# Optimization experiments

Measured on AMD Instinct MI355X. Metric: run time of the kernel, lower is better.

The kernel has to match this reference:

```python
import jax, jax.numpy as jnp
from jax import lax
import numpy as np

B, L, D = 2048, 100, 64      # batch, max_len, embedding_dim
K = 64                       # embedding_num (codebook entries)
CB = K * 8                   # code_book_dim = 512 (== D*8 encoder out channels)
ITEMS = 1_000_000
EPS = 1e-3                   # tf.layers.batch_normalization default epsilon


def setup_inputs() -> dict:
    key = jax.random.key(0)
    ks = jax.random.split(key, 16)
    w = lambda i, shape: jax.random.normal(ks[i], shape, dtype=jnp.float32) * 0.05
    z = lambda c: jnp.zeros((c,), jnp.float32)
    o = lambda c: jnp.ones((c,), jnp.float32)
    return {
        "history_item_ids": jax.random.randint(ks[0], (B, L), 0, ITEMS, dtype=jnp.int32),
        "history_item_masks": jax.random.randint(ks[1], (B, L), 0, 2, dtype=jnp.int32),
        "item_embedding_table": jax.random.normal(ks[2], (ITEMS, D), dtype=jnp.float32),
        "user_book": jax.random.normal(ks[3], (K, CB), dtype=jnp.float32),
        "e_w1": w(4, (2, 2, D, 2 * D)), "e_b1": z(2 * D), "e_g1": o(2 * D), "e_be1": z(2 * D),
        "e_w2": w(5, (2, 2, 2 * D, 4 * D)), "e_b2": z(4 * D), "e_g2": o(4 * D), "e_be2": z(4 * D),
        "e_w3": w(6, (2, 2, 4 * D, 8 * D)), "e_b3": z(8 * D),
        "d_w1": w(7, (2, 2, 8 * D, 4 * D)), "d_b1": z(4 * D), "d_g1": o(4 * D), "d_be1": z(4 * D),
        "d_w2": w(8, (2, 2, 4 * D, 2 * D)), "d_b2": z(2 * D), "d_g2": o(2 * D), "d_be2": z(2 * D),
        "d_w3": w(9, (2, 2, 2 * D, D)), "d_b3": z(D),
    }


def _forward(history_item_ids, history_item_masks, item_embedding_table, user_book,
             e_w1, e_b1, e_g1, e_be1, e_w2, e_b2, e_g2, e_be2, e_w3, e_b3,
             d_w1, d_b1, d_g1, d_be1, d_w2, d_b2, d_g2, d_be2, d_w3, d_b3):
    dn = ('NHWC', 'HWIO', 'NHWC')
    bn = lambda x, g, b: x * (g / jnp.sqrt(1.0 + EPS)) + b  # inference BN: moving mean 0, var 1
    conv = lambda x, w_, b_: lax.conv_general_dilated(x, w_, (1, 1), 'VALID', dimension_numbers=dn) + b_
    deconv = lambda x, w_, b_: lax.conv_transpose(x, w_, (1, 1), 'VALID', dimension_numbers=dn) + b_

    mask = (history_item_masks >= 1).astype(jnp.float32)               # [B,L]
    hist = item_embedding_table[history_item_ids] * mask[..., None]    # [B,L,D]

    H = int(L ** 0.5); W = L // H
    h = hist.reshape(-1, H, W, D)
    h = jax.nn.relu(bn(conv(h, e_w1, e_b1), e_g1, e_be1))              # [B,9,9,2D]
    h = jax.nn.relu(bn(conv(h, e_w2, e_b2), e_g2, e_be2))              # [B,8,8,4D]
    x_encode = conv(h, e_w3, e_b3)                                     # [B,7,7,CB]

    # nearest-neighbor codebook lookup (get_quantized)
    flat = x_encode.reshape(-1, CB)                                    # [B*49,CB]
    dist = ((flat * flat).sum(1, keepdims=True)
            + (user_book * user_book).sum(1)
            - 2.0 * flat @ user_book.T)                                # [B*49,K]
    idx = jnp.argmin(dist, axis=1)
    quantized = user_book[idx].reshape(x_encode.shape)                 # [B,7,7,CB]

    # straight-through estimator
    st = x_encode + lax.stop_gradient(quantized - x_encode)
    g = jax.nn.relu(bn(deconv(st, d_w1, d_b1), d_g1, d_be1))           # [B,8,8,4D]
    g = jax.nn.relu(bn(deconv(g, d_w2, d_b2), d_g2, d_be2))            # [B,9,9,2D]
    vq_x = deconv(g, d_w3, d_b3).reshape(hist.shape)                   # [B,L,D]

    vq_mean = vq_x.sum(1) / mask.sum(-1, keepdims=True)                # [B,D]
    mse = lambda a, b: jnp.mean((a - b) ** 2)
    beta = 0.25
    vqvae_loss = (mse(hist, vq_x)
                  + mse(quantized, lax.stop_gradient(x_encode))
                  + beta * mse(x_encode, lax.stop_gradient(quantized)))
    return vq_mean, vq_x, vqvae_loss


def reference(history_item_ids, history_item_masks, item_embedding_table, user_book,
              e_w1, e_b1, e_g1, e_be1, e_w2, e_b2, e_g2, e_be2, e_w3, e_b3,
              d_w1, d_b1, d_g1, d_be1, d_w2, d_b2, d_g2, d_be2, d_w3, d_b3):
    return _forward(history_item_ids, history_item_masks, item_embedding_table, user_book,
                    e_w1, e_b1, e_g1, e_be1, e_w2, e_b2, e_g2, e_be2, e_w3, e_b3,
                    d_w1, d_b1, d_g1, d_be1, d_w2, d_b2, d_g2, d_be2, d_w3, d_b3)
```

## Files before the change

kernel.cpp:

```cpp
#include <hip/hip_runtime.h>
#include <hip/hip_bf16.h>
#include <cstdint>
#include <cstddef>


typedef __attribute__((ext_vector_type(8))) short short8v;
typedef __attribute__((ext_vector_type(4))) float f32x4;

constexpr int B  = 2048;
constexpr int L  = 100;
constexpr int K  = 64;
constexpr int CB = 512;
#define MARGIN 0.1f

constexpr size_t R0_OFF  = 0;
constexpr size_t R1_OFF  = 51380224;
constexpr size_t IDX_OFF = 84934656;
constexpr size_t CBN_OFF = 85035008;
constexpr size_t CNT_OFF = 85035072;
constexpr size_t ACC_OFF = 85035088;
constexpr size_t WL_OFF  = 85035104;
constexpr size_t WB_OFF  = 85135456;

constexpr size_t EW1H=0,       EW1L=32768;
constexpr size_t EW2H=65536,   EW2L=196608;
constexpr size_t EW3H=327680;
constexpr size_t DW2H=851968,  DW3H=983040;
constexpr size_t W3BH=1015808, W3BL=1081344;

constexpr size_t BW1_OFF  = WB_OFF + 573440;
constexpr size_t DOTB_OFF = BW1_OFF + 65536;

__device__ inline ushort bf16_hi(float f){ __hip_bfloat16 h=__float2bfloat16(f); return *(ushort*)&h; }
__device__ inline float  bf16_tof(ushort u){ __hip_bfloat16 h; *(ushort*)&h=u; return __bfloat162float(h); }

__device__ void wtrans(const float* __restrict__ w, int IC, int OC,
                       ushort* __restrict__ hi, ushort* __restrict__ lo,
                       int gid, int gsz)
{
    int tot = 4*IC*OC;
    for (int i = gid; i < tot; i += gsz) {
        int kk = i/(IC*OC), r = i - kk*(IC*OC), ic = r/OC, oc = r - ic*OC;
        float v = w[i];
        ushort h = bf16_hi(v);
        size_t dst = ((size_t)kk*OC + oc)*IC + ic;
        hi[dst] = h;
        if (lo) lo[dst] = bf16_hi(v - bf16_tof(h));
    }
}

__global__ __launch_bounds__(256)
void wprep_k(const float* e1, const float* e2, const float* e3,
             const float* d2, const float* d3, ushort* wb)
{
    int gid = blockIdx.x*256 + threadIdx.x, gsz = gridDim.x*256;
    wtrans(e1,  64, 128, wb+EW1H, wb+EW1L, gid, gsz);
    wtrans(e2, 128, 256, wb+EW2H, wb+EW2L, gid, gsz);
    wtrans(e3, 256, 512, wb+EW3H, nullptr, gid, gsz);
    wtrans(d2, 256, 128, wb+DW2H, nullptr, gid, gsz);
    wtrans(d3, 128,  64, wb+DW3H, nullptr, gid, gsz);
}

__global__ __launch_bounds__(256)
void w3b_k(const float* __restrict__ e_w3, const float* __restrict__ book,
           ushort* __restrict__ wb)
{
    const int kk = blockIdx.x >> 6, k = blockIdx.x & 63, ic = threadIdx.x;
    const float4* wr = (const float4*)(e_w3 + ((size_t)(kk*256)+ic)*512);
    const float4* br = (const float4*)(book + (size_t)k*512);
    float s = 0.f;
    for (int c = 0; c < 128; ++c) {
        float4 a = wr[c], bb = br[c];
        s = fmaf(a.x,bb.x,fmaf(a.y,bb.y,fmaf(a.z,bb.z,fmaf(a.w,bb.w,s))));
    }
    size_t dst = ((size_t)(kk*64+k))*256 + ic;
    ushort h = bf16_hi(s);
    wb[W3BH+dst] = h;
    wb[W3BL+dst] = bf16_hi(s - bf16_tof(h));
}

__global__ __launch_bounds__(256)
void bw1_k(const float* __restrict__ d_w1, const float* __restrict__ book,
           float* __restrict__ bw1)
{
    const int tap = blockIdx.x >> 6, k = blockIdx.x & 63, oc = threadIdx.x;
    const float* br = book + (size_t)k*512;
    const float* wr = d_w1 + (size_t)(tap*512)*256 + oc;
    float s = 0.f;
    for (int ic = 0; ic < 512; ++ic)
        s = fmaf(br[ic], wr[(size_t)ic*256], s);
    bw1[((size_t)(tap*64+k))*256 + oc] = s;
}

__global__ __launch_bounds__(256)
void prep_k(const float* __restrict__ book, const float* __restrict__ e_b3,
            float* __restrict__ cbn, float* __restrict__ dotb,
            float* __restrict__ acc, int* __restrict__ cnt)
{
    const int t = threadIdx.x;
    if (t < 64) {
        const float* r = book + t * 512;
        float s = 0.f, d = 0.f;
        for (int c = 0; c < 512; ++c) { s = fmaf(r[c], r[c], s); d = fmaf(e_b3[c], r[c], d); }
        cbn[t] = s; dotb[t] = d;
    }
    if (t == 64 || t == 65) acc[t-64] = 0.f;
    if (t == 66) *cnt = 0;
}

template<int IH,int IW,int IC,int OC,int PAD,int MODE,bool HASBN,bool SPLIT,
         int OCS,int ICC,int MT,int OUTFMT,bool FUSE,int SMP,bool DBUF>
__global__ __launch_bounds__(256)
void sconv_k(const uint* __restrict__ in_pk, const ushort* __restrict__ in_bf,
             const int* __restrict__ ids, const int* __restrict__ masks,
             const float* __restrict__ table,
             const ushort* __restrict__ wt_hi, const ushort* __restrict__ wt_lo,
             const float* __restrict__ bias, const float* __restrict__ gamma,
             const float* __restrict__ beta,
             float* __restrict__ out_f, uint* __restrict__ out_pk,
             ushort* __restrict__ out_bf, float* __restrict__ out_mean,
             float* __restrict__ acc_g)
{
    constexpr int OH=IH+2*PAD-1, OW=IW+2*PAD-1, NPOS=OH*OW, IHW=IH*IW;
    constexpr int OCB=OC/OCS, NPW=OCB/4, NT=NPW/16;
    constexpr int NCH=IC/ICC, KS=ICC/32;
    constexpr int PL=SPLIT?2:1;
    constexpr int NB=(DBUF && NCH>1)?2:1;
    constexpr int AROWS=IHW+1, RB=ICC*2;
    constexpr int C8=ICC/8;
    constexpr int NITEMS=SMP*IHW*C8;
    constexpr int SI=(NITEMS+255)/256;
    constexpr bool EXACT=(SI*256==NITEMS);
    constexpr int SPLB=AROWS*RB;
    constexpr int SAMB=PL*SPLB;
    constexpr int BUFB=SMP*SAMB;

    __shared__ ushort s_a[NB*SMP*PL*AROWS*ICC];
    char* sb=(char*)s_a;

    const int v=blockIdx.x, r8=v&7, iv=v>>3;
    const int b0 = (r8*(B/SMP/8) + iv/OCS)*SMP;
    const int sl = iv - (iv/OCS)*OCS;

    const int tid=threadIdx.x, lane=tid&63, wv=tid>>6;
    const int l15=lane&15, lq=lane>>4;
    const int n0=sl*OCB + wv*NPW;

    int arow[4][MT];
    #pragma unroll
    for(int kk=0;kk<4;++kk){
        const int ky=kk>>1, kx=kk&1;
        #pragma unroll
        for(int m=0;m<MT;++m){
            int p=m*16+l15;
            int py=p/OW, px=p-py*OW;
            int ty=py+ky-PAD, tx=px+kx-PAD;
            bool ok=(p<NPOS)&&((unsigned)ty<(unsigned)IH)&&((unsigned)tx<(unsigned)IW);
            arow[kk][m]= ok ? ty*IW+tx : IHW;
        }
    }

    f32x4 acc[SMP][MT][NT];
    #pragma unroll
    for(int s=0;s<SMP;++s)
        #pragma unroll
        for(int m=0;m<MT;++m)
            #pragma unroll
            for(int n=0;n<NT;++n) acc[s][m][n]=(f32x4)0.0f;

    uint4 r0[SI];
    uint4 r1[(MODE==1||MODE==3)?SI:1];
    float msk[(MODE==1)?SI:1];

    auto stage_load=[&](int c){
        const int ic0=c*ICC;
        #pragma unroll
        for(int t=0;t<SI;++t){
            int idx=tid+t*256;
            if(EXACT || idx<NITEMS){
                int row=idx/C8, g=idx-row*C8;
                int s=row/IHW, r=row-s*IHW;
                if constexpr(MODE==1){
                    int id=ids[(b0+s)*L+r];
                    msk[t]=(masks[(b0+s)*L+r]>=1)?1.f:0.f;
                    const float* src=table+(size_t)id*64+g*8;
                    r0[t]=*(const uint4*)src;
                    r1[t]=*(const uint4*)(src+4);
                } else if constexpr(MODE==3){
                    const uint* src=in_pk+((size_t)(b0+s)*IHW+r)*IC+ic0+g*8;
                    r0[t]=*(const uint4*)src;
                    r1[t]=*(const uint4*)(src+4);
                } else {
                    r0[t]=*(const uint4*)(in_bf+((size_t)(b0+s)*IHW+r)*IC+ic0+g*8);
                }
            }
        }
    };

    auto stage_write=[&](int bufb){
        #pragma unroll
        for(int t=0;t<SI;++t){
            int idx=tid+t*256;
            if(EXACT || idx<NITEMS){
                int row=idx/C8, g=idx-row*C8;
                int s=row/IHW, r=row-s*IHW;
                int boff=bufb + s*SAMB + r*RB + ((g^(r&7))<<4);
                if constexpr(MODE==1){
                    const float* f0=(const float*)&r0[t];
                    const float* f1=(const float*)&r1[t];
                    float vv[8]={f0[0]*msk[t],f0[1]*msk[t],f0[2]*msk[t],f0[3]*msk[t],
                                 f1[0]*msk[t],f1[1]*msk[t],f1[2]*msk[t],f1[3]*msk[t]};
                    ushort hh[8], ll[8];
                    #pragma unroll
                    for(int j=0;j<8;++j){ hh[j]=bf16_hi(vv[j]); ll[j]=bf16_hi(vv[j]-bf16_tof(hh[j])); }
                    *(uint4*)(sb+boff)=*(uint4*)hh;
                    *(uint4*)(sb+SPLB+boff)=*(uint4*)ll;
                } else if constexpr(MODE==3){
                    const uint* u0=(const uint*)&r0[t];
                    const uint* u1=(const uint*)&r1[t];
                    ushort hh[8], ll[8];
                    #pragma unroll
                    for(int j=0;j<4;++j){ hh[j]=(ushort)(u0[j]&0xffffu); ll[j]=(ushort)(u0[j]>>16); }
                    #pragma unroll
                    for(int j=0;j<4;++j){ hh[4+j]=(ushort)(u1[j]&0xffffu); ll[4+j]=(ushort)(u1[j]>>16); }
                    *(uint4*)(sb+boff)=*(uint4*)hh;
                    *(uint4*)(sb+SPLB+boff)=*(uint4*)ll;
                } else {
                    *(uint4*)(sb+boff)=r0[t];
                }
            }
        }
    };

    auto zero_rows=[&](){
        for(int z=tid; z<NB*SMP*PL*C8; z+=256){
            int nb=z/(SMP*PL*C8), rz=z-nb*(SMP*PL*C8);
            int s=rz/(PL*C8), rz2=rz-s*(PL*C8), pl=rz2/C8, g=rz2-pl*C8;
            *(uint4*)(sb + nb*BUFB + s*SAMB + pl*SPLB + IHW*RB + (g<<4)) = make_uint4(0,0,0,0);
        }
    };

    auto do_mfma=[&](int bufb, int c){
        const int ic0=c*ICC;
        __builtin_amdgcn_s_setprio(1);
        #pragma unroll
        for(int kk=0;kk<4;++kk){
            #pragma unroll
            for(int ks=0;ks<KS;++ks){
                short8v bhv[NT]; short8v blv[SPLIT?NT:1];
                #pragma unroll
                for(int n=0;n<NT;++n){
                    int col=n0+n*16+l15;
                    size_t widx=((size_t)kk*OC+col)*IC+ic0+ks*32+lq*8;
                    bhv[n]=*(const short8v*)(wt_hi+widx);
                    if constexpr(SPLIT) blv[n]=*(const short8v*)(wt_lo+widx);
                }
                #pragma unroll
                for(int s=0;s<SMP;++s){
                    const int sbase=bufb + s*SAMB;
                    #pragma unroll
                    for(int m=0;m<MT;++m){
                        int off=sbase + arow[kk][m]*RB + ((((ks<<2)|lq)^(arow[kk][m]&7))<<4);
                        short8v ah=*(const short8v*)(sb+off);
                        if constexpr(SPLIT){
                            short8v al=*(const short8v*)(sb+SPLB+off);
                            #pragma unroll
                            for(int n=0;n<NT;++n){
                                acc[s][m][n]=__builtin_amdgcn_mfma_f32_16x16x32_bf16(ah,bhv[n],acc[s][m][n],0,0,0);
                                acc[s][m][n]=__builtin_amdgcn_mfma_f32_16x16x32_bf16(ah,blv[n],acc[s][m][n],0,0,0);
                                acc[s][m][n]=__builtin_amdgcn_mfma_f32_16x16x32_bf16(al,bhv[n],acc[s][m][n],0,0,0);
                            }
                        } else {
                            #pragma unroll
                            for(int n=0;n<NT;++n)
                                acc[s][m][n]=__builtin_amdgcn_mfma_f32_16x16x32_bf16(ah,bhv[n],acc[s][m][n],0,0,0);
                        }
                    }
                }
            }
        }
        __builtin_amdgcn_s_setprio(0);
    };

    if constexpr(NB==1){
        stage_load(0);
        zero_rows();
        for(int c=0;c<NCH;++c){
            if(c) __syncthreads();
            stage_write(0);
            __syncthreads();
            if(c+1<NCH) stage_load(c+1);
            do_mfma(0,c);
        }
    } else {
        stage_load(0);
        stage_write(0);
        zero_rows();
        __syncthreads();
        for(int c=0;c<NCH;++c){
            if(c+1<NCH) stage_load(c+1);
            do_mfma((c&1)*BUFB,c);
            if(c+1<NCH){
                stage_write(((c+1)&1)*BUFB);
                __syncthreads();
            }
        }
    }

    const float rs=(float)(1.0/sqrt(1.0+1e-3));
    float lsum=0.f, colsum=0.f;
    #pragma unroll
    for(int s=0;s<SMP;++s){
        const int b=b0+s;
        #pragma unroll
        for(int n=0;n<NT;++n){
            int col=n0+n*16+l15;
            float bi=bias[col];
            float gsc=0.f, bt=0.f;
            if constexpr(HASBN){ gsc=gamma[col]*rs; bt=beta[col]; }
            #pragma unroll
            for(int m=0;m<MT;++m){
                #pragma unroll
                for(int j=0;j<4;++j){
                    int p=m*16+lq*4+j;
                    if(p<NPOS){
                        float vx=acc[s][m][n][j]+bi;
                        if constexpr(HASBN) vx=fmaxf(fmaf(vx,gsc,bt),0.f);
                        size_t g=(size_t)b*NPOS+p;
                        if constexpr(OUTFMT==0){
                            out_f[g*OC+col]=vx;
                        } else if constexpr(OUTFMT==1){
                            ushort h=bf16_hi(vx);
                            ushort lo=bf16_hi(vx-bf16_tof(h));
                            out_pk[g*OC+col]=(uint)h | ((uint)lo<<16);
                        } else {
                            out_bf[g*OC+col]=bf16_hi(vx);
                        }
                        if constexpr(FUSE){
                            int id=ids[b*L+p];
                            float mm=(masks[b*L+p]>=1)?1.f:0.f;
                            float h=table[(size_t)id*64+col]*mm;
                            float df=h-vx;
                            lsum=fmaf(df,df,lsum);
                            colsum+=vx;
                        }
                    }
                }
            }
        }
    }

    if constexpr(FUSE){
        const int b=b0;
        float mc=0.f;
        for(int l=lane;l<L;l+=64) mc += (masks[b*L+l]>=1)?1.f:0.f;
        #pragma unroll
        for(int off=32;off;off>>=1) mc+=__shfl_xor(mc,off);
        colsum += __shfl_xor(colsum,16);
        colsum += __shfl_xor(colsum,32);
        if(lq==0) out_mean[b*64 + n0 + l15] = colsum/mc;
        #pragma unroll
        for(int off=32;off;off>>=1) lsum+=__shfl_xor(lsum,off);
        __syncthreads();
        float* red=(float*)sb;
        if(lane==0) red[wv]=lsum;
        __syncthreads();
        if(tid==0) atomicAdd(acc_g+0, red[0]+red[1]+red[2]+red[3]);
    }
}

__device__ inline int xswz(int row, int sl){ return (sl ^ (row&31) ^ ((row>>3)&7)) << 4; }

__global__ __launch_bounds__(512)
void xnd4_k(const uint* __restrict__ in_pk,
            const ushort* __restrict__ wx,
            const ushort* __restrict__ w3bh, const ushort* __restrict__ w3bl,
            const float* __restrict__ xbias,
            const float* __restrict__ cbn, const float* __restrict__ dotb,
            int* __restrict__ qidx, float* __restrict__ acc_g,
            int* __restrict__ cnt, int* __restrict__ wl)
{
    constexpr int NPOS=49, OW=7, MT=4;
    constexpr int ROWB=512;
    constexpr int PLB=64*ROWB;

    __shared__ ushort s_a[2*64*256];
    char* sb=(char*)s_a;

    const int v=blockIdx.x;
    const int b=(v&7)*(B/8)+(v>>3);
    const int tid=threadIdx.x, lane=tid&63, wv=tid>>6;
    const int l15=lane&15, lq=lane>>4;

    #pragma unroll
    for(int t=0;t<4;++t){
        int idx=tid+t*512;
        int row=idx>>5, sl=idx&31;
        const uint* src=in_pk+((size_t)b*64+row)*256+sl*8;
        uint4 u0=*(const uint4*)src, u1=*(const uint4*)(src+4);
        const uint* p0=(const uint*)&u0;
        const uint* p1=(const uint*)&u1;
        ushort hh[8], ll[8];
        #pragma unroll
        for(int j=0;j<4;++j){ hh[j]=(ushort)(p0[j]&0xffffu); ll[j]=(ushort)(p0[j]>>16); }
        #pragma unroll
        for(int j=0;j<4;++j){ hh[4+j]=(ushort)(p1[j]&0xffffu); ll[4+j]=(ushort)(p1[j]>>16); }
        int boff=row*ROWB+xswz(row,sl);
        *(uint4*)(sb+boff)=*(uint4*)hh;
        *(uint4*)(sb+PLB+boff)=*(uint4*)ll;
    }
    __syncthreads();

    int arow[4][MT];
    #pragma unroll
    for(int kk=0;kk<4;++kk){
        const int ky=kk>>1, kx=kk&1;
        #pragma unroll
        for(int m=0;m<MT;++m){
            int p=m*16+l15;
            int py=p/OW, px=p-py*OW;
            arow[kk][m]= (p<NPOS) ? (py+ky)*8+(px+kx) : 0;
        }
    }

    f32x4 accd[MT];
    #pragma unroll
    for(int m=0;m<MT;++m) accd[m]=(f32x4)0.0f;
    if(wv<4){
        __builtin_amdgcn_s_setprio(1);
        #pragma unroll
        for(int kk=0;kk<4;++kk){
            #pragma unroll
            for(int ks=0;ks<8;++ks){
                int cold=wv*16+l15;
                size_t wdx=((size_t)kk*64+cold)*256+ks*32+lq*8;
                short8v bdh=*(const short8v*)(w3bh+wdx);
                short8v bdl=*(const short8v*)(w3bl+wdx);
                const int slb=ks*4+lq;
                #pragma unroll
                for(int m=0;m<MT;++m){
                    int r=arow[kk][m];
                    int off=r*ROWB+xswz(r,slb);
                    short8v ah=*(const short8v*)(sb+off);
                    short8v al=*(const short8v*)(sb+PLB+off);
                    accd[m]=__builtin_amdgcn_mfma_f32_16x16x32_bf16(ah,bdh,accd[m],0,0,0);
                    accd[m]=__builtin_amdgcn_mfma_f32_16x16x32_bf16(ah,bdl,accd[m],0,0,0);
                    accd[m]=__builtin_amdgcn_mfma_f32_16x16x32_bf16(al,bdh,accd[m],0,0,0);
                }
            }
        }
        __builtin_amdgcn_s_setprio(0);
    }

    float xs=0.f;
    #pragma unroll
    for(int cc=0;cc<2;++cc){
        f32x4 accx[MT][2];
        #pragma unroll
        for(int m=0;m<MT;++m){ accx[m][0]=(f32x4)0.0f; accx[m][1]=(f32x4)0.0f; }
        const int col0=wv*64+cc*32+l15;
        __builtin_amdgcn_s_setprio(1);
        #pragma unroll
        for(int kk=0;kk<4;++kk){
            #pragma unroll
            for(int ks=0;ks<8;++ks){
                short8v bx0=*(const short8v*)(wx+((size_t)kk*512+col0)*256+ks*32+lq*8);
                short8v bx1=*(const short8v*)(wx+((size_t)kk*512+col0+16)*256+ks*32+lq*8);
                const int slb=ks*4+lq;
                #pragma unroll
                for(int m=0;m<MT;++m){
                    int r=arow[kk][m];
                    int off=r*ROWB+xswz(r,slb);
                    short8v ah=*(const short8v*)(sb+off);
                    accx[m][0]=__builtin_amdgcn_mfma_f32_16x16x32_bf16(ah,bx0,accx[m][0],0,0,0);
                    accx[m][1]=__builtin_amdgcn_mfma_f32_16x16x32_bf16(ah,bx1,accx[m][1],0,0,0);
                }
            }
        }
        __builtin_amdgcn_s_setprio(0);
        #pragma unroll
        for(int n=0;n<2;++n){
            const float bi=xbias[col0+n*16];
            #pragma unroll
            for(int m=0;m<MT;++m){
                #pragma unroll
                for(int j=0;j<4;++j){
                    int p=m*16+lq*4+j;
                    if(p<NPOS){ float vv=accx[m][n][j]+bi; xs=fmaf(vv,vv,xs); }
                }
            }
        }
    }
    #pragma unroll
    for(int off=32;off;off>>=1) xs+=__shfl_xor(xs,off);

    __syncthreads();
    float* f=(float*)sb;
    if(lane==0) f[wv]=xs;

    float* sd1=f+16;
    int*   sk =(int*)(f+16+256);
    float* sd2=f+16+512;
    if(wv<4){
        float cb=cbn[wv*16+l15], db=dotb[wv*16+l15];
        #pragma unroll
        for(int m=0;m<MT;++m){
            #pragma unroll
            for(int j=0;j<4;++j){
                int p=m*16+lq*4+j;
                float d1=cb-2.f*(accd[m][j]+db);
                int   k1=wv*16+l15;
                float d2=3.4e38f;
                #pragma unroll
                for(int off=1;off<16;off<<=1){
                    float od1=__shfl_xor(d1,off);
                    int   ok1=__shfl_xor(k1,off);
                    float od2=__shfl_xor(d2,off);
                    if(od1<d1 || (od1==d1 && ok1<k1)){ d2=fminf(d1,od2); d1=od1; k1=ok1; }
                    else                              { d2=fminf(d2,od1); }
                }
                if(l15==0 && p<NPOS){ sd1[p*4+wv]=d1; sk[p*4+wv]=k1; sd2[p*4+wv]=d2; }
            }
        }
    }
    __syncthreads();
    if(tid==0) atomicAdd(acc_g+1, f[0]+f[1]+f[2]+f[3]+f[4]+f[5]+f[6]+f[7]);

    {
        float lsum=0.f;
        if(tid<NPOS){
            float d1=sd1[tid*4+0]; int k1=sk[tid*4+0]; float d2=sd2[tid*4+0];
            #pragma unroll
            for(int w=1;w<4;++w){
                float D1=sd1[tid*4+w]; int K1=sk[tid*4+w]; float D2=sd2[tid*4+w];
                if(D1<d1){ d2=fminf(d1,D2); d1=D1; k1=K1; }
                else     { d2=fminf(d2,D1); }
            }
            qidx[b*49+tid]=k1;
            if(d2-d1<=MARGIN){ int t=atomicAdd(cnt,1); wl[t]=b*49+tid; }
            lsum=d1;
        }
        if(tid<64){
            #pragma unroll
            for(int off=32;off;off>>=1) lsum+=__shfl_xor(lsum,off);
            if(tid==0) atomicAdd(acc_g+1, lsum);
        }
    }
}

__global__ __launch_bounds__(256)
void dgather_k(const int* __restrict__ qidx, const float* __restrict__ bw1,
               const float* __restrict__ b1, const float* __restrict__ g1s,
               const float* __restrict__ be1, ushort* __restrict__ G1)
{
    const int b=blockIdx.x, tid=threadIdx.x;
    const int pg=tid>>2, og=(tid&3)*64;
    const int py=pg>>3, px=pg&7;

    float a[64];
    #pragma unroll
    for(int j=0;j<64;++j) a[j]=0.f;

    #pragma unroll
    for(int tap=0;tap<4;++tap){
        int iy=py+(tap>>1)-1, ix=px+(tap&1)-1;
        if((unsigned)iy<7u && (unsigned)ix<7u){
            int kq=qidx[b*49+iy*7+ix];
            const float4* src=(const float4*)(bw1+((size_t)(tap*64+kq))*256+og);
            #pragma unroll
            for(int j=0;j<16;++j){
                float4 vv=src[j];
                a[4*j+0]+=vv.x; a[4*j+1]+=vv.y; a[4*j+2]+=vv.z; a[4*j+3]+=vv.w;
            }
        }
    }
    const float rs=(float)(1.0/sqrt(1.0+1e-3));
    #pragma unroll
    for(int j=0;j<64;++j){
        int col=og+j;
        float vv=a[j]+b1[col];
        vv=fmaxf(fmaf(vv, g1s[col]*rs, be1[col]), 0.f);
        G1[((size_t)b*64+pg)*256+col]=bf16_hi(vv);
    }
}

__global__ __launch_bounds__(256)
void recompute_k(const int* __restrict__ wl, const int* __restrict__ cnt,
                 const int* __restrict__ ids, const int* __restrict__ masks,
                 const float* __restrict__ table, const float* __restrict__ book,
                 const float* __restrict__ e_w1, const float* __restrict__ e_b1,
                 const float* __restrict__ e_g1, const float* __restrict__ e_be1,
                 const float* __restrict__ e_w2, const float* __restrict__ e_b2,
                 const float* __restrict__ e_g2, const float* __restrict__ e_be2,
                 const float* __restrict__ e_w3, const float* __restrict__ e_b3,
                 int* __restrict__ qidx)
{
    __shared__ double s_h[16*64];
    __shared__ double s_a1[9*128];
    __shared__ double s_a2[4*256];
    __shared__ double s_x[512];
    __shared__ double s_d[256];

    const int tid = threadIdx.x;
    const double rs = 1.0 / sqrt(1.0 + 1e-3);
    const int n = *cnt;

    for (int wi = blockIdx.x; wi < n; wi += gridDim.x) {
        const int row = wl[wi];
        const int b = row / 49, p = row % 49;
        const int py = p / 7, px = p % 7;

        for (int i = tid; i < 16*64; i += 256) {
            int cell = i >> 6, d = i & 63;
            int l = (py + (cell >> 2)) * 10 + (px + (cell & 3));
            int id = ids[b*100 + l];
            double m = (masks[b*100 + l] >= 1) ? 1.0 : 0.0;
            s_h[i] = (double)table[(size_t)id*64 + d] * m;
        }
        __syncthreads();

        for (int i = tid; i < 9*128; i += 256) {
            int cell = i >> 7, oc = i & 127;
            int ry = cell / 3, rx = cell % 3;
            double s = 0.0;
            #pragma unroll
            for (int kk = 0; kk < 4; ++kk) {
                int icell = (ry + (kk>>1))*4 + (rx + (kk&1));
                const double* hh = s_h + icell*64;
                const float* ww = e_w1 + (kk*64)*128 + oc;
                for (int ic = 0; ic < 64; ++ic)
                    s = fma(hh[ic], (double)ww[ic*128], s);
            }
            s += (double)e_b1[oc];
            s = s * ((double)e_g1[oc] * rs) + (double)e_be1[oc];
            s_a1[i] = s > 0.0 ? s : 0.0;
        }
        __syncthreads();

        for (int i = tid; i < 4*256; i += 256) {
            int cell = i >> 8, oc = i & 255;
            int qy = cell >> 1, qx = cell & 1;
            double s = 0.0;
            #pragma unroll
            for (int kk = 0; kk < 4; ++kk) {
                int icell = (qy + (kk>>1))*3 + (qx + (kk&1));
                const double* aa = s_a1 + icell*128;
                const float* ww = e_w2 + (kk*128)*256 + oc;
                for (int ic = 0; ic < 128; ++ic)
                    s = fma(aa[ic], (double)ww[ic*256], s);
            }
            s += (double)e_b2[oc];
            s = s * ((double)e_g2[oc] * rs) + (double)e_be2[oc];
            s_a2[i] = s > 0.0 ? s : 0.0;
        }
        __syncthreads();

        for (int i = tid; i < 512; i += 256) {
            double s = 0.0;
            #pragma unroll
            for (int kk = 0; kk < 4; ++kk) {
                const double* aa = s_a2 + kk*256;
                const float* ww = e_w3 + (kk*256)*512 + i;
                for (int ic = 0; ic < 256; ++ic)
                    s = fma(aa[ic], (double)ww[ic*512], s);
            }
            s_x[i] = s + (double)e_b3[i];
        }
        __syncthreads();

        {
            int k = tid & 63, seg = tid >> 6;
            const float* cr = book + k*512 + seg*128;
            const double* xr = s_x + seg*128;
            double s = 0.0;
            for (int c = 0; c < 128; ++c) {
                double dd = xr[c] - (double)cr[c];
                s = fma(dd, dd, s);
            }
            s_d[seg*64 + k] = s;
        }
        __syncthreads();

        if (tid < 64) {
            double dv = s_d[tid] + s_d[64+tid] + s_d[128+tid] + s_d[192+tid];
            int kk2 = tid;
            #pragma unroll
            for (int off = 32; off > 0; off >>= 1) {
                double od = __shfl_xor(dv, off);
                int    ok = __shfl_xor(kk2, off);
                if (od < dv || (od == dv && ok < kk2)) { dv = od; kk2 = ok; }
            }
            if (tid == 0) qidx[row] = kk2;
        }
        __syncthreads();
    }
}

__global__ void loss_k(const float* __restrict__ acc, float* __restrict__ out_loss)
{
    float l1 = acc[0] / 13107200.f;
    float l2 = acc[1] / 51380224.f;
    out_loss[0] = l1 + l2 + 0.25f * l2;
}

extern "C" void kernel_launch(void* const* d_in, const int* in_sizes, int n_in,
                              void* d_out, int out_size, void* d_ws, size_t ws_size,
                              hipStream_t stream)
{
    const int*   ids   = (const int*)d_in[0];
    const int*   masks = (const int*)d_in[1];
    const float* table = (const float*)d_in[2];
    const float* book  = (const float*)d_in[3];
    const float* e_w1  = (const float*)d_in[4];
    const float* e_b1  = (const float*)d_in[5];
    const float* e_g1  = (const float*)d_in[6];
    const float* e_be1 = (const float*)d_in[7];
    const float* e_w2  = (const float*)d_in[8];
    const float* e_b2  = (const float*)d_in[9];
    const float* e_g2  = (const float*)d_in[10];
    const float* e_be2 = (const float*)d_in[11];
    const float* e_w3  = (const float*)d_in[12];
    const float* e_b3  = (const float*)d_in[13];
    const float* d_w1  = (const float*)d_in[14];
    const float* d_b1  = (const float*)d_in[15];
    const float* d_g1  = (const float*)d_in[16];
    const float* d_be1 = (const float*)d_in[17];
    const float* d_w2  = (const float*)d_in[18];
    const float* d_b2  = (const float*)d_in[19];
    const float* d_g2  = (const float*)d_in[20];
    const float* d_be2 = (const float*)d_in[21];
    const float* d_w3  = (const float*)d_in[22];
    const float* d_b3  = (const float*)d_in[23];

    float*  ws  = (float*)d_ws;
    uint*   A1P = (uint*)(ws + R0_OFF);
    uint*   A2P = (uint*)(ws + R1_OFF);
    ushort* G1  = (ushort*)(ws + R1_OFF);
    ushort* G2  = (ushort*)(ws + R0_OFF);
    int*    IDX = (int*)(ws + IDX_OFF);
    float*  CBN = ws + CBN_OFF;
    int*    CNT = (int*)(ws + CNT_OFF);
    float*  ACC = ws + ACC_OFF;
    int*    WL  = (int*)(ws + WL_OFF);
    ushort* WB  = (ushort*)(ws + WB_OFF);
    float*  BW1 = ws + BW1_OFF;
    float*  DOTB= ws + DOTB_OFF;

    float* out_mean = (float*)d_out;
    float* out_vqx  = (float*)d_out + (size_t)B * 64;
    float* out_loss = (float*)d_out + (size_t)B * 64 + (size_t)B * L * 64;

    prep_k<<<1, 256, 0, stream>>>(book, e_b3, CBN, DOTB, ACC, CNT);
    wprep_k<<<512, 256, 0, stream>>>(e_w1, e_w2, e_w3, d_w2, d_w3, WB);
    w3b_k<<<256, 256, 0, stream>>>(e_w3, book, WB);
    bw1_k<<<256, 256, 0, stream>>>(d_w1, book, BW1);

    sconv_k<10,10, 64,128,0,1,true ,true ,1, 64,6,1,false,1,true ><<<B,   256,0,stream>>>(
        nullptr, nullptr, ids, masks, table,
        WB+EW1H, WB+EW1L, e_b1, e_g1, e_be1, nullptr, A1P, nullptr, nullptr, nullptr);
    sconv_k< 9, 9,128,256,0,3,true ,true ,2, 64,4,1,false,1,true ><<<B*2, 256,0,stream>>>(
        A1P, nullptr, nullptr, nullptr, nullptr,
        WB+EW2H, WB+EW2L, e_b2, e_g2, e_be2, nullptr, A2P, nullptr, nullptr, nullptr);

    xnd4_k<<<B, 512, 0, stream>>>(A2P, WB+EW3H, WB+W3BH, WB+W3BL,
                                  e_b3, CBN, DOTB, IDX, ACC, CNT, WL);

    recompute_k<<<512, 256, 0, stream>>>(WL, CNT, ids, masks, table, book,
                                         e_w1, e_b1, e_g1, e_be1,
                                         e_w2, e_b2, e_g2, e_be2,
                                         e_w3, e_b3, IDX);

    dgather_k<<<B, 256, 0, stream>>>(IDX, BW1, d_b1, d_g1, d_be1, G1);
    sconv_k< 8, 8,256,128,1,4,true ,false,1, 64,6,2,false,1,true ><<<B,   256,0,stream>>>(
        nullptr, G1, nullptr, nullptr, nullptr,
        WB+DW2H, nullptr, d_b2, d_g2, d_be2, nullptr, nullptr, G2, nullptr, nullptr);
    sconv_k< 9, 9,128, 64,1,4,false,false,1, 64,7,0,true ,1,true ><<<B,   256,0,stream>>>(
        nullptr, G2, ids, masks, table,
        WB+DW3H, nullptr, d_b3, nullptr, nullptr, out_vqx, nullptr, nullptr, out_mean, ACC);

    loss_k<<<1, 1, 0, stream>>>(ACC, out_loss);
}
```

Baseline: 1.165 ms.

## Split fused encoder-3/quantize kernel into separate x-square and codebook-distance kernels

The fused kernel, in which only four of eight waves computed codebook dot products while all eight did the x-squared sum, is split into two kernels. The x-squared kernel loads only the high bf16 plane, using half the LDS. The distance kernel spreads the K dimension across all eight waves and reduces the partial sums through LDS. This is meant to balance wave work and lower LDS pressure, at the cost of a second launch and of reading the activation input twice from global memory.

```diff
diff --git a/kernel.cpp b/kernel.cpp
--- a/kernel.cpp
+++ b/kernel.cpp
@@ -372,13 +372,103 @@
 __device__ inline int xswz(int row, int sl){ return (sl ^ (row&31) ^ ((row>>3)&7)) << 4; }
 
 __global__ __launch_bounds__(512)
-void xnd4_k(const uint* __restrict__ in_pk,
-            const ushort* __restrict__ wx,
-            const ushort* __restrict__ w3bh, const ushort* __restrict__ w3bl,
-            const float* __restrict__ xbias,
-            const float* __restrict__ cbn, const float* __restrict__ dotb,
-            int* __restrict__ qidx, float* __restrict__ acc_g,
-            int* __restrict__ cnt, int* __restrict__ wl)
+void xsq_k(const uint* __restrict__ in_pk,
+           const ushort* __restrict__ wx,
+           const float* __restrict__ xbias,
+           float* __restrict__ acc_g)
+{
+    constexpr int NPOS=49, OW=7, MT=4;
+    constexpr int ROWB=512;
+
+    __shared__ ushort s_a[64*256];
+    char* sb=(char*)s_a;
+
+    const int v=blockIdx.x;
+    const int b=(v&7)*(B/8)+(v>>3);
+    const int tid=threadIdx.x, lane=tid&63, wv=tid>>6;
+    const int l15=lane&15, lq=lane>>4;
+
+    #pragma unroll
+    for(int t=0;t<4;++t){
+        int idx=tid+t*512;
+        int row=idx>>5, sl=idx&31;
+        const uint* src=in_pk+((size_t)b*64+row)*256+sl*8;
+        uint4 u0=*(const uint4*)src, u1=*(const uint4*)(src+4);
+        const uint* p0=(const uint*)&u0;
+        const uint* p1=(const uint*)&u1;
+        ushort hh[8];
+        #pragma unroll
+        for(int j=0;j<4;++j){ hh[j]=(ushort)(p0[j]&0xffffu); hh[4+j]=(ushort)(p1[j]&0xffffu); }
+        *(uint4*)(sb+row*ROWB+xswz(row,sl))=*(uint4*)hh;
+    }
+    __syncthreads();
+
+    int arow[4][MT];
+    #pragma unroll
+    for(int kk=0;kk<4;++kk){
+        const int ky=kk>>1, kx=kk&1;
+        #pragma unroll
+        for(int m=0;m<MT;++m){
+            int p=m*16+l15;
+            int py=p/OW, px=p-py*OW;
+            arow[kk][m]= (p<NPOS) ? (py+ky)*8+(px+kx) : 0;
+        }
+    }
+
+    float xs=0.f;
+    #pragma unroll
+    for(int cc=0;cc<2;++cc){
+        f32x4 accx[MT][2];
+        #pragma unroll
+        for(int m=0;m<MT;++m){ accx[m][0]=(f32x4)0.0f; accx[m][1]=(f32x4)0.0f; }
+        const int col0=wv*64+cc*32+l15;
+        __builtin_amdgcn_s_setprio(1);
+        #pragma unroll
+        for(int kk=0;kk<4;++kk){
+            #pragma unroll
+            for(int ks=0;ks<8;++ks){
+                short8v bx0=*(const short8v*)(wx+((size_t)kk*512+col0)*256+ks*32+lq*8);
+                short8v bx1=*(const short8v*)(wx+((size_t)kk*512+col0+16)*256+ks*32+lq*8);
+                const int slb=ks*4+lq;
+                #pragma unroll
+                for(int m=0;m<MT;++m){
+                    int r=arow[kk][m];
+                    short8v ah=*(const short8v*)(sb+r*ROWB+xswz(r,slb));
+                    accx[m][0]=__builtin_amdgcn_mfma_f32_16x16x32_bf16(ah,bx0,accx[m][0],0,0,0);
+                    accx[m][1]=__builtin_amdgcn_mfma_f32_16x16x32_bf16(ah,bx1,accx[m][1],0,0,0);
+                }
+            }
+        }
+        __builtin_amdgcn_s_setprio(0);
+        #pragma unroll
+        for(int n=0;n<2;++n){
+            const float bi=xbias[col0+n*16];
+            #pragma unroll
+            for(int m=0;m<MT;++m){
+                #pragma unroll
+                for(int j=0;j<4;++j){
+                    int p=m*16+lq*4+j;
+                    if(p<NPOS){ float vv=accx[m][n][j]+bi; xs=fmaf(vv,vv,xs); }
+                }
+            }
+        }
+    }
+    #pragma unroll
+    for(int off=32;off;off>>=1) xs+=__shfl_xor(xs,off);
+
+    __syncthreads();
+    float* f=(float*)sb;
+    if(lane==0) f[wv]=xs;
+    __syncthreads();
+    if(tid==0) atomicAdd(acc_g+1, f[0]+f[1]+f[2]+f[3]+f[4]+f[5]+f[6]+f[7]);
+}
+
+__global__ __launch_bounds__(512)
+void dot_k(const uint* __restrict__ in_pk,
+           const ushort* __restrict__ w3bh, const ushort* __restrict__ w3bl,
+           const float* __restrict__ cbn, const float* __restrict__ dotb,
+           int* __restrict__ qidx, float* __restrict__ acc_g,
+           int* __restrict__ cnt, int* __restrict__ wl)
 {
     constexpr int NPOS=49, OW=7, MT=4;
     constexpr int ROWB=512;
@@ -423,93 +513,62 @@
         }
     }
 
+    const int cold=(wv&3)*16+l15;
+    const int ks0=(wv>>2)*4;
     f32x4 accd[MT];
     #pragma unroll
     for(int m=0;m<MT;++m) accd[m]=(f32x4)0.0f;
-    if(wv<4){
-        __builtin_amdgcn_s_setprio(1);
-        #pragma unroll
-        for(int kk=0;kk<4;++kk){
-            #pragma unroll
-            for(int ks=0;ks<8;++ks){
-                int cold=wv*16+l15;
-                size_t wdx=((size_t)kk*64+cold)*256+ks*32+lq*8;
-                short8v bdh=*(const short8v*)(w3bh+wdx);
-                short8v bdl=*(const short8v*)(w3bl+wdx);
-                const int slb=ks*4+lq;
-                #pragma unroll
-                for(int m=0;m<MT;++m){
-                    int r=arow[kk][m];
-                    int off=r*ROWB+xswz(r,slb);
-                    short8v ah=*(const short8v*)(sb+off);
-                    short8v al=*(const short8v*)(sb+PLB+off);
-                    accd[m]=__builtin_amdgcn_mfma_f32_16x16x32_bf16(ah,bdh,accd[m],0,0,0);
-                    accd[m]=__builtin_amdgcn_mfma_f32_16x16x32_bf16(ah,bdl,accd[m],0,0,0);
-                    accd[m]=__builtin_amdgcn_mfma_f32_16x16x32_bf16(al,bdh,accd[m],0,0,0);
-                }
-            }
-        }
-        __builtin_amdgcn_s_setprio(0);
-    }
-
-    float xs=0.f;
-    #pragma unroll
-    for(int cc=0;cc<2;++cc){
-        f32x4 accx[MT][2];
-        #pragma unroll
-        for(int m=0;m<MT;++m){ accx[m][0]=(f32x4)0.0f; accx[m][1]=(f32x4)0.0f; }
-        const int col0=wv*64+cc*32+l15;
-        __builtin_amdgcn_s_setprio(1);
-        #pragma unroll
-        for(int kk=0;kk<4;++kk){
-            #pragma unroll
-            for(int ks=0;ks<8;++ks){
-                short8v bx0=*(const short8v*)(wx+((size_t)kk*512+col0)*256+ks*32+lq*8);
-                short8v bx1=*(const short8v*)(wx+((size_t)kk*512+col0+16)*256+ks*32+lq*8);
-                const int slb=ks*4+lq;
-                #pragma unroll
-                for(int m=0;m<MT;++m){
-                    int r=arow[kk][m];
-                    int off=r*ROWB+xswz(r,slb);
-                    short8v ah=*(const short8v*)(sb+off);
-                    accx[m][0]=__builtin_amdgcn_mfma_f32_16x16x32_bf16(ah,bx0,accx[m][0],0,0,0);
-                    accx[m][1]=__builtin_amdgcn_mfma_f32_16x16x32_bf16(ah,bx1,accx[m][1],0,0,0);
-                }
-            }
-        }
-        __builtin_amdgcn_s_setprio(0);
-        #pragma unroll
-        for(int n=0;n<2;++n){
-            const float bi=xbias[col0+n*16];
+
+    __builtin_amdgcn_s_setprio(1);
+    #pragma unroll
+    for(int kk=0;kk<4;++kk){
+        #pragma unroll
+        for(int kq2=0;kq2<4;++kq2){
+            const int ks=ks0+kq2;
+            size_t wdx=((size_t)kk*64+cold)*256+ks*32+lq*8;
+            short8v bdh=*(const short8v*)(w3bh+wdx);
+            short8v bdl=*(const short8v*)(w3bl+wdx);
+            const int slb=ks*4+lq;
             #pragma unroll
             for(int m=0;m<MT;++m){
-                #pragma unroll
-                for(int j=0;j<4;++j){
-                    int p=m*16+lq*4+j;
-                    if(p<NPOS){ float vv=accx[m][n][j]+bi; xs=fmaf(vv,vv,xs); }
-                }
-            }
-        }
-    }
-    #pragma unroll
-    for(int off=32;off;off>>=1) xs+=__shfl_xor(xs,off);
+                int r=arow[kk][m];
+                int off=r*ROWB+xswz(r,slb);
+                short8v ah=*(const short8v*)(sb+off);
+                short8v al=*(const short8v*)(sb+PLB+off);
+                accd[m]=__builtin_amdgcn_mfma_f32_16x16x32_bf16(ah,bdh,accd[m],0,0,0);
+                accd[m]=__builtin_amdgcn_mfma_f32_16x16x32_bf16(ah,bdl,accd[m],0,0,0);
+                accd[m]=__builtin_amdgcn_mfma_f32_16x16x32_bf16(al,bdh,accd[m],0,0,0);
+            }
+        }
+    }
+    __builtin_amdgcn_s_setprio(0);
 
     __syncthreads();
     float* f=(float*)sb;
-    if(lane==0) f[wv]=xs;
-
-    float* sd1=f+16;
-    int*   sk =(int*)(f+16+256);
-    float* sd2=f+16+512;
+    if(wv>=4){
+        float* dst=f+((wv-4)*64+lane)*16;
+        #pragma unroll
+        for(int m=0;m<MT;++m){
+            #pragma unroll
+            for(int j=0;j<4;++j) dst[m*4+j]=accd[m][j];
+        }
+    }
+    __syncthreads();
+
+    float* sd1=f+4096;
+    int*   sk =(int*)(f+4096+256);
+    float* sd2=f+4096+512;
     if(wv<4){
-        float cb=cbn[wv*16+l15], db=dotb[wv*16+l15];
+        const float* srcp=f+(wv*64+lane)*16;
+        float cb=cbn[cold], db=dotb[cold];
         #pragma unroll
         for(int m=0;m<MT;++m){
             #pragma unroll
             for(int j=0;j<4;++j){
                 int p=m*16+lq*4+j;
-                float d1=cb-2.f*(accd[m][j]+db);
-                int   k1=wv*16+l15;
+                float dtot=accd[m][j]+srcp[m*4+j];
+                float d1=cb-2.f*(dtot+db);
+                int   k1=cold;
                 float d2=3.4e38f;
                 #pragma unroll
                 for(int off=1;off<16;off<<=1){
@@ -524,7 +583,6 @@
         }
     }
     __syncthreads();
-    if(tid==0) atomicAdd(acc_g+1, f[0]+f[1]+f[2]+f[3]+f[4]+f[5]+f[6]+f[7]);
 
     {
         float lsum=0.f;
@@ -762,8 +820,8 @@
         A1P, nullptr, nullptr, nullptr, nullptr,
         WB+EW2H, WB+EW2L, e_b2, e_g2, e_be2, nullptr, A2P, nullptr, nullptr, nullptr);
 
-    xnd4_k<<<B, 512, 0, stream>>>(A2P, WB+EW3H, WB+W3BH, WB+W3BL,
-                                  e_b3, CBN, DOTB, IDX, ACC, CNT, WL);
+    xsq_k<<<B, 512, 0, stream>>>(A2P, WB+EW3H, e_b3, ACC);
+    dot_k<<<B, 512, 0, stream>>>(A2P, WB+W3BH, WB+W3BL, CBN, DOTB, IDX, ACC, CNT, WL);
 
     recompute_k<<<512, 256, 0, stream>>>(WL, CNT, ids, masks, table, book,
                                          e_w1, e_b1, e_g1, e_be1,
```

Measured after the change: 1.149 ms. No clear change (-1.4%).
